# Optimization experiments

Hardware: AMD Instinct MI355X
Metric: run time of the kernel (lower is better)

## Reference

```python
import jax, jax.numpy as jnp
import numpy as np

N, D, K = 40000, 64, 16
E = N * K
EPS = 1e-5  # torch BatchNorm1d default eps


def _bn(h, g, b):
    # BatchNorm1d in training mode: biased batch statistics over dim 0
    m = h.mean(0)
    v = h.var(0)
    return (h - m) * jax.lax.rsqrt(v + EPS) * g + b


def setup_inputs() -> dict:
    key = jax.random.key(0)
    ks = jax.random.split(key, 4)
    kp = jax.random.split(ks[3], 9)

    def w(k, shape):
        return (jax.random.normal(k, shape, dtype=jnp.float32) / np.float32(np.sqrt(shape[0])))

    src = jax.random.randint(ks[2], (E,), 0, N, dtype=jnp.int32)
    dst = jnp.repeat(jnp.arange(N, dtype=jnp.int32), K)  # kNN-style: each node has K in-edges

    return {
        "x": jax.random.normal(ks[0], (N, D), dtype=jnp.float32),
        "pos": jax.random.normal(ks[1], (N, 3), dtype=jnp.float32),
        "edge_index": jnp.stack([src, dst]),
        "W_in": w(kp[0], (D, D)),
        "g1": jnp.ones(D), "b1": jnp.zeros(D),
        "W_v": w(kp[1], (D, D)),
        "W_src": w(kp[2], (D, D)),
        "W_dst": w(kp[3], (D, D)),
        "Wp1": w(kp[4], (3, 3)), "bp1": jnp.zeros(3),
        "gp": jnp.ones(3), "bp": jnp.zeros(3),
        "Wp2": w(kp[5], (3, D)), "bp2": jnp.zeros(D),
        "ga0": jnp.ones(D), "ba0": jnp.zeros(D),
        "Wa1": w(kp[6], (D, D // 8)), "ba1": jnp.zeros(D // 8),
        "ga1": jnp.ones(D // 8), "bb1": jnp.zeros(D // 8),
        "Wa2": w(kp[7], (D // 8, D)), "ba2": jnp.zeros(D),
        "g2": jnp.ones(D), "b2": jnp.zeros(D),
        "W_out": w(kp[8], (D, D)),
        "g3": jnp.ones(D), "b3": jnp.zeros(D),
    }


def reference(x, pos, edge_index, W_in, g1, b1, W_v, W_src, W_dst,
              Wp1, bp1, gp, bp, Wp2, bp2, ga0, ba0, Wa1, ba1, ga1, bb1,
              Wa2, ba2, g2, b2, W_out, g3, b3):
    src, dst = edge_index[0], edge_index[1]  # j (source), i (dest)
    n = x.shape[0]
    x_skip = x
    h = jax.nn.relu(_bn(x @ W_in, g1, b1))

    # PointTransformerConv
    a_src = h @ W_src            # alpha_j projection [N,D]
    a_dst = h @ W_dst            # alpha_i projection [N,D]
    v = h @ W_v                  # value projection  [N,D]
    rel = pos[dst] - pos[src]    # pos_i - pos_j     [E,3]
    ph = jax.nn.relu(_bn(rel @ Wp1 + bp1, gp, bp))
    delta = ph @ Wp2 + bp2       # pos_nn output     [E,D]
    a = a_dst[dst] - a_src[src] + delta
    # attn_nn: BN -> ReLU -> (Lin+BN+ReLU) -> Lin
    a = jax.nn.relu(_bn(a, ga0, ba0))
    a = jax.nn.relu(_bn(a @ Wa1 + ba1, ga1, bb1))
    a = a @ Wa2 + ba2            # [E,D]
    # segment-wise softmax over incoming edges of each dest node
    amax = jax.lax.stop_gradient(jax.ops.segment_max(a, dst, num_segments=n))
    e = jnp.exp(a - amax[dst])
    s = jax.ops.segment_sum(e, dst, num_segments=n)
    attn = e / (s[dst] + 1e-16)  # PyG softmax adds 1e-16
    agg = jax.ops.segment_sum(attn * (v[src] + delta), dst, num_segments=n)

    h = jax.nn.relu(_bn(agg, g2, b2))
    h = _bn(h @ W_out, g3, b3)
    return jax.nn.relu(h + x_skip)
```

## Files before the change

kernel.cpp:

```cpp
#include <hip/hip_runtime.h>

#define NN 40000
#define DDIM 64
#define KE 16
#define EE 640000
#define BNEPS 1e-5f

__device__ __forceinline__ void bn_coeff(const float* __restrict__ S, int C, int c,
                                         const float* __restrict__ g, const float* __restrict__ b,
                                         float inv_n, float& sc, float& sh)
{
    float m   = S[c] * inv_n;
    float var = S[C + c] * inv_n - m * m;
    float r   = rsqrtf(var + BNEPS);
    sc = g[c] * r;
    sh = b[c] - m * sc;
}

template<int TRN>
__global__ __launch_bounds__(256) void gemm64_k(
    const float* __restrict__ in,
    const float* __restrict__ W0, const float* __restrict__ W1, const float* __restrict__ W2,
    float* __restrict__ out0, float* __restrict__ out1, float* __restrict__ out2,
    const float* __restrict__ Sin, const float* __restrict__ gamma, const float* __restrict__ beta,
    float inv_n, float* __restrict__ Sout)
{
    const float* W = (blockIdx.y == 0) ? W0 : ((blockIdx.y == 1) ? W1 : W2);
    float* out     = (blockIdx.y == 0) ? out0 : ((blockIdx.y == 1) ? out1 : out2);

    __shared__ float Wl[64][64];
    __shared__ float inl[64][65];
    __shared__ float scl[64], shl[64];
    __shared__ float ssum[64], ssq[64];

    const int t = threadIdx.x;
    if (t < 64) {
        if (TRN) { float sc, sh; bn_coeff(Sin, 64, t, gamma, beta, inv_n, sc, sh); scl[t] = sc; shl[t] = sh; }
        ssum[t] = 0.f; ssq[t] = 0.f;
    }
#pragma unroll
    for (int i = 0; i < 16; i++) { int idx = t + i * 256; Wl[idx >> 6][idx & 63] = W[idx]; }
    __syncthreads();

    const int rbase = blockIdx.x * 64;
    {
        const int d = t & 63;
        float sc = 0.f, sh = 0.f;
        if (TRN) { sc = scl[d]; sh = shl[d]; }
#pragma unroll
        for (int i = 0; i < 16; i++) {
            int r = (t >> 6) + i * 4;
            float v = in[(size_t)(rbase + r) * 64 + d];
            if (TRN) v = fmaxf(fmaf(v, sc, sh), 0.f);
            inl[r][d] = v;
        }
    }
    __syncthreads();

    const int c0 = (t & 15) * 4, r0 = (t >> 4) * 4;
    float acc[4][4] = {};
#pragma unroll 16
    for (int d = 0; d < 64; d++) {
        float4 w4 = *(const float4*)&Wl[d][c0];
#pragma unroll
        for (int i = 0; i < 4; i++) {
            float h = inl[r0 + i][d];
            acc[i][0] = fmaf(h, w4.x, acc[i][0]);
            acc[i][1] = fmaf(h, w4.y, acc[i][1]);
            acc[i][2] = fmaf(h, w4.z, acc[i][2]);
            acc[i][3] = fmaf(h, w4.w, acc[i][3]);
        }
    }
#pragma unroll
    for (int i = 0; i < 4; i++) {
        float4 o; o.x = acc[i][0]; o.y = acc[i][1]; o.z = acc[i][2]; o.w = acc[i][3];
        *(float4*)&out[(size_t)(rbase + r0 + i) * 64 + c0] = o;
    }
    if (Sout) {
#pragma unroll
        for (int j = 0; j < 4; j++) {
            float s  = acc[0][j] + acc[1][j] + acc[2][j] + acc[3][j];
            float qv = acc[0][j] * acc[0][j] + acc[1][j] * acc[1][j] + acc[2][j] * acc[2][j] + acc[3][j] * acc[3][j];
            atomicAdd(&ssum[c0 + j], s);
            atomicAdd(&ssq[c0 + j], qv);
        }
        __syncthreads();
        if (t < 64) { atomicAdd(&Sout[t], ssum[t]); atomicAdd(&Sout[64 + t], ssq[t]); }
    }
}

__global__ __launch_bounds__(256) void edge_q_k(
    const float* __restrict__ pos, const int* __restrict__ src,
    const float* __restrict__ Wp1, const float* __restrict__ bp1,
    float4* __restrict__ q4, float* __restrict__ Sq)
{
    float w00 = Wp1[0], w01 = Wp1[1], w02 = Wp1[2];
    float w10 = Wp1[3], w11 = Wp1[4], w12 = Wp1[5];
    float w20 = Wp1[6], w21 = Wp1[7], w22 = Wp1[8];
    float c0 = bp1[0], c1 = bp1[1], c2 = bp1[2];
    float s0 = 0, s1 = 0, s2 = 0, p0 = 0, p1 = 0, p2 = 0;
    for (int e = blockIdx.x * blockDim.x + threadIdx.x; e < EE; e += gridDim.x * blockDim.x) {
        int sj = src[e]; int di = e >> 4;
        float r0 = pos[di * 3 + 0] - pos[sj * 3 + 0];
        float r1 = pos[di * 3 + 1] - pos[sj * 3 + 1];
        float r2 = pos[di * 3 + 2] - pos[sj * 3 + 2];
        float v0 = c0 + r0 * w00 + r1 * w10 + r2 * w20;
        float v1 = c1 + r0 * w01 + r1 * w11 + r2 * w21;
        float v2 = c2 + r0 * w02 + r1 * w12 + r2 * w22;
        float4 o; o.x = v0; o.y = v1; o.z = v2; o.w = __int_as_float(sj);
        q4[e] = o;
        s0 += v0; s1 += v1; s2 += v2;
        p0 += v0 * v0; p1 += v1 * v1; p2 += v2 * v2;
    }
#pragma unroll
    for (int o = 32; o > 0; o >>= 1) {
        s0 += __shfl_down(s0, o); s1 += __shfl_down(s1, o); s2 += __shfl_down(s2, o);
        p0 += __shfl_down(p0, o); p1 += __shfl_down(p1, o); p2 += __shfl_down(p2, o);
    }
    __shared__ float sred[4][6];
    const int w = threadIdx.x >> 6;
    if ((threadIdx.x & 63) == 0) {
        sred[w][0] = s0; sred[w][1] = s1; sred[w][2] = s2;
        sred[w][3] = p0; sred[w][4] = p1; sred[w][5] = p2;
    }
    __syncthreads();
    if (threadIdx.x < 6) {
        float v = sred[0][threadIdx.x] + sred[1][threadIdx.x] + sred[2][threadIdx.x] + sred[3][threadIdx.x];
        atomicAdd(&Sq[threadIdx.x], v);
    }
}

__global__ __launch_bounds__(256) void edge_a0_k(
    const float4* __restrict__ q4v,
    const float* __restrict__ adst, const float* __restrict__ asrc,
    const float* __restrict__ Wp2, const float* __restrict__ bp2,
    const float* __restrict__ Sq, const float* __restrict__ gp, const float* __restrict__ bp_,
    float* __restrict__ Sa0)
{
    const int lane = threadIdx.x & 63;
    const int r = lane >> 4, fq = lane & 15;
    const int wv   = blockIdx.x * (blockDim.x >> 6) + (threadIdx.x >> 6);
    const int nwv  = gridDim.x * (blockDim.x >> 6);
    const float inv_e = 1.0f / (float)EE;
    float sc30, sh30, sc31, sh31, sc32, sh32;
    bn_coeff(Sq, 3, 0, gp, bp_, inv_e, sc30, sh30);
    bn_coeff(Sq, 3, 1, gp, bp_, inv_e, sc31, sh31);
    bn_coeff(Sq, 3, 2, gp, bp_, inv_e, sc32, sh32);
    float4 w0_4 = *(const float4*)&Wp2[fq * 4];
    float4 w1_4 = *(const float4*)&Wp2[64 + fq * 4];
    float4 w2_4 = *(const float4*)&Wp2[128 + fq * 4];
    float4 bd4  = *(const float4*)&bp2[fq * 4];
    float4 s4 = {0.f,0.f,0.f,0.f}, p4 = {0.f,0.f,0.f,0.f};

    for (int i = wv; i < NN; i += nwv) {
        const int e0 = i << 4;
        float4 ad4 = *(const float4*)&adst[(size_t)i * 64 + fq * 4];
        float4 qs  = q4v[e0 + (lane & 15)];
        int sv = __float_as_int(qs.w);
        int sj[4];
#pragma unroll
        for (int p = 0; p < 4; p++) sj[p] = __shfl(sv, p * 4 + r);
        float4 av[4];
#pragma unroll
        for (int p = 0; p < 4; p++) av[p] = *(const float4*)&asrc[(size_t)sj[p] * 64 + fq * 4];
#pragma unroll
        for (int p = 0; p < 4; p++) {
            int j = p * 4 + r;
            float ph0 = fmaxf(fmaf(__shfl(qs.x, j), sc30, sh30), 0.f);
            float ph1 = fmaxf(fmaf(__shfl(qs.y, j), sc31, sh31), 0.f);
            float ph2 = fmaxf(fmaf(__shfl(qs.z, j), sc32, sh32), 0.f);
            float4 a0v;
            a0v.x = ad4.x - av[p].x + bd4.x + ph0 * w0_4.x + ph1 * w1_4.x + ph2 * w2_4.x;
            a0v.y = ad4.y - av[p].y + bd4.y + ph0 * w0_4.y + ph1 * w1_4.y + ph2 * w2_4.y;
            a0v.z = ad4.z - av[p].z + bd4.z + ph0 * w0_4.z + ph1 * w1_4.z + ph2 * w2_4.z;
            a0v.w = ad4.w - av[p].w + bd4.w + ph0 * w0_4.w + ph1 * w1_4.w + ph2 * w2_4.w;
            s4.x += a0v.x; s4.y += a0v.y; s4.z += a0v.z; s4.w += a0v.w;
            p4.x = fmaf(a0v.x, a0v.x, p4.x); p4.y = fmaf(a0v.y, a0v.y, p4.y);
            p4.z = fmaf(a0v.z, a0v.z, p4.z); p4.w = fmaf(a0v.w, a0v.w, p4.w);
        }
    }
    s4.x += __shfl_xor(s4.x, 16); s4.y += __shfl_xor(s4.y, 16);
    s4.z += __shfl_xor(s4.z, 16); s4.w += __shfl_xor(s4.w, 16);
    p4.x += __shfl_xor(p4.x, 16); p4.y += __shfl_xor(p4.y, 16);
    p4.z += __shfl_xor(p4.z, 16); p4.w += __shfl_xor(p4.w, 16);
    s4.x += __shfl_xor(s4.x, 32); s4.y += __shfl_xor(s4.y, 32);
    s4.z += __shfl_xor(s4.z, 32); s4.w += __shfl_xor(s4.w, 32);
    p4.x += __shfl_xor(p4.x, 32); p4.y += __shfl_xor(p4.y, 32);
    p4.z += __shfl_xor(p4.z, 32); p4.w += __shfl_xor(p4.w, 32);

    __shared__ float ls[64], lq[64];
    if (threadIdx.x < 64) { ls[threadIdx.x] = 0.f; lq[threadIdx.x] = 0.f; }
    __syncthreads();
    if (lane < 16) {
        atomicAdd(&ls[fq * 4 + 0], s4.x); atomicAdd(&ls[fq * 4 + 1], s4.y);
        atomicAdd(&ls[fq * 4 + 2], s4.z); atomicAdd(&ls[fq * 4 + 3], s4.w);
        atomicAdd(&lq[fq * 4 + 0], p4.x); atomicAdd(&lq[fq * 4 + 1], p4.y);
        atomicAdd(&lq[fq * 4 + 2], p4.z); atomicAdd(&lq[fq * 4 + 3], p4.w);
    }
    __syncthreads();
    if (threadIdx.x < 64) { atomicAdd(&Sa0[threadIdx.x], ls[threadIdx.x]); atomicAdd(&Sa0[64 + threadIdx.x], lq[threadIdx.x]); }
}

__global__ __launch_bounds__(256) void edge_t_k(
    const float4* __restrict__ q4v,
    const float* __restrict__ adst, const float* __restrict__ asrc,
    const float* __restrict__ Wp2, const float* __restrict__ bp2,
    const float* __restrict__ Sq, const float* __restrict__ gp, const float* __restrict__ bp_,
    const float* __restrict__ Sa0, const float* __restrict__ ga0, const float* __restrict__ ba0,
    const float* __restrict__ Wa1, const float* __restrict__ ba1,
    float* __restrict__ tout, float* __restrict__ St)
{
    __shared__ float t_l[4][16][8];
    __shared__ float red[16];
    const int t = threadIdx.x, lane = t & 63, w = t >> 6;
    const int r = lane >> 4, fq = lane & 15;
    const int wv  = blockIdx.x * 4 + w;
    const int nwv = gridDim.x * 4;
    const float inv_e = 1.0f / (float)EE;
    float sc30, sh30, sc31, sh31, sc32, sh32;
    bn_coeff(Sq, 3, 0, gp, bp_, inv_e, sc30, sh30);
    bn_coeff(Sq, 3, 1, gp, bp_, inv_e, sc31, sh31);
    bn_coeff(Sq, 3, 2, gp, bp_, inv_e, sc32, sh32);
    float4 scA4, shA4;
    bn_coeff(Sa0, 64, fq * 4 + 0, ga0, ba0, inv_e, scA4.x, shA4.x);
    bn_coeff(Sa0, 64, fq * 4 + 1, ga0, ba0, inv_e, scA4.y, shA4.y);
    bn_coeff(Sa0, 64, fq * 4 + 2, ga0, ba0, inv_e, scA4.z, shA4.z);
    bn_coeff(Sa0, 64, fq * 4 + 3, ga0, ba0, inv_e, scA4.w, shA4.w);
    float4 w0_4 = *(const float4*)&Wp2[fq * 4];
    float4 w1_4 = *(const float4*)&Wp2[64 + fq * 4];
    float4 w2_4 = *(const float4*)&Wp2[128 + fq * 4];
    float4 bd4  = *(const float4*)&bp2[fq * 4];
    float wAf[4][8];
#pragma unroll
    for (int d = 0; d < 4; d++) {
        float4 lo = *(const float4*)&Wa1[(size_t)(fq * 4 + d) * 8];
        float4 hi = *(const float4*)&Wa1[(size_t)(fq * 4 + d) * 8 + 4];
        wAf[d][0] = lo.x; wAf[d][1] = lo.y; wAf[d][2] = lo.z; wAf[d][3] = lo.w;
        wAf[d][4] = hi.x; wAf[d][5] = hi.y; wAf[d][6] = hi.z; wAf[d][7] = hi.w;
    }
    float bb[8];
    {
        float4 lo = *(const float4*)&ba1[0];
        float4 hi = *(const float4*)&ba1[4];
        bb[0] = lo.x; bb[1] = lo.y; bb[2] = lo.z; bb[3] = lo.w;
        bb[4] = hi.x; bb[5] = hi.y; bb[6] = hi.z; bb[7] = hi.w;
    }
    float ss[8] = {}, sp[8] = {};
    if (t < 16) red[t] = 0.f;
    __syncthreads();

    for (int i = wv; i < NN; i += nwv) {
        const int e0 = i << 4;
        float4 ad4 = *(const float4*)&adst[(size_t)i * 64 + fq * 4];
        float4 qs  = q4v[e0 + (lane & 15)];
        int sv = __float_as_int(qs.w);
        int sj[4];
#pragma unroll
        for (int p = 0; p < 4; p++) sj[p] = __shfl(sv, p * 4 + r);
        float4 av[4];
#pragma unroll
        for (int p = 0; p < 4; p++) av[p] = *(const float4*)&asrc[(size_t)sj[p] * 64 + fq * 4];
#pragma unroll
        for (int p = 0; p < 4; p++) {
            int j = p * 4 + r;
            float ph0 = fmaxf(fmaf(__shfl(qs.x, j), sc30, sh30), 0.f);
            float ph1 = fmaxf(fmaf(__shfl(qs.y, j), sc31, sh31), 0.f);
            float ph2 = fmaxf(fmaf(__shfl(qs.z, j), sc32, sh32), 0.f);
            float4 a1v;
            a1v.x = ad4.x - av[p].x + bd4.x + ph0 * w0_4.x + ph1 * w1_4.x + ph2 * w2_4.x;
            a1v.y = ad4.y - av[p].y + bd4.y + ph0 * w0_4.y + ph1 * w1_4.y + ph2 * w2_4.y;
            a1v.z = ad4.z - av[p].z + bd4.z + ph0 * w0_4.z + ph1 * w1_4.z + ph2 * w2_4.z;
            a1v.w = ad4.w - av[p].w + bd4.w + ph0 * w0_4.w + ph1 * w1_4.w + ph2 * w2_4.w;
            a1v.x = fmaxf(fmaf(a1v.x, scA4.x, shA4.x), 0.f);
            a1v.y = fmaxf(fmaf(a1v.y, scA4.y, shA4.y), 0.f);
            a1v.z = fmaxf(fmaf(a1v.z, scA4.z, shA4.z), 0.f);
            a1v.w = fmaxf(fmaf(a1v.w, scA4.w, shA4.w), 0.f);
            float part[8];
#pragma unroll
            for (int k = 0; k < 8; k++) {
                part[k] = a1v.x * wAf[0][k] + a1v.y * wAf[1][k]
                        + a1v.z * wAf[2][k] + a1v.w * wAf[3][k];
            }
#pragma unroll
            for (int k = 0; k < 8; k++) {
                part[k] += __shfl_xor(part[k], 1);
                part[k] += __shfl_xor(part[k], 2);
                part[k] += __shfl_xor(part[k], 4);
                part[k] += __shfl_xor(part[k], 8);
            }
            if (fq == 0) {
#pragma unroll
                for (int k = 0; k < 8; k++) {
                    float v = part[k] + bb[k];
                    t_l[w][p * 4 + r][k] = v;
                    ss[k] += v; sp[k] = fmaf(v, v, sp[k]);
                }
            }
        }
        float2 o = *(const float2*)&t_l[w][lane >> 2][(lane & 3) * 2];
        *(float2*)&tout[(size_t)e0 * 8 + lane * 2] = o;
    }
#pragma unroll
    for (int k = 0; k < 8; k++) {
        ss[k] += __shfl_xor(ss[k], 16); ss[k] += __shfl_xor(ss[k], 32);
        sp[k] += __shfl_xor(sp[k], 16); sp[k] += __shfl_xor(sp[k], 32);
    }
    if (lane == 0) {
#pragma unroll
        for (int k = 0; k < 8; k++) { atomicAdd(&red[k], ss[k]); atomicAdd(&red[8 + k], sp[k]); }
    }
    __syncthreads();
    if (t < 16) atomicAdd(&St[t], red[t]);
}

__global__ __launch_bounds__(256) void edge_final_k(
    const float* __restrict__ tin,
    const float4* __restrict__ q4v, const float* __restrict__ vv,
    const float* __restrict__ Wp2, const float* __restrict__ bp2,
    const float* __restrict__ Sq, const float* __restrict__ gp, const float* __restrict__ bp_,
    const float* __restrict__ St, const float* __restrict__ ga1, const float* __restrict__ bb1,
    const float* __restrict__ Wa2, const float* __restrict__ ba2,
    float* __restrict__ agg, float* __restrict__ Sagg)
{
    __shared__ float att_l[4][16][68];
    __shared__ float tt_l[4][16][8];
    __shared__ float ls[64], lq[64];
    const int t = threadIdx.x, lane = t & 63, w = t >> 6;
    const int r = lane >> 4, fq = lane & 15;
    const float inv_e = 1.0f / (float)EE;
    float sc3[3], sh3[3];
#pragma unroll
    for (int k = 0; k < 3; k++) bn_coeff(Sq, 3, k, gp, bp_, inv_e, sc3[k], sh3[k]);
    float sc8[8], sh8[8];
#pragma unroll
    for (int k = 0; k < 8; k++) bn_coeff(St, 8, k, ga1, bb1, inv_e, sc8[k], sh8[k]);
    float wa[8];
#pragma unroll
    for (int k = 0; k < 8; k++) wa[k] = Wa2[k * 64 + lane];
    float bad = ba2[lane];
    float4 wp0_4 = *(const float4*)&Wp2[fq * 4];
    float4 wp1_4 = *(const float4*)&Wp2[64 + fq * 4];
    float4 wp2_4 = *(const float4*)&Wp2[128 + fq * 4];
    float4 bpd4  = *(const float4*)&bp2[fq * 4];
    float4 ssum4 = {0.f, 0.f, 0.f, 0.f}, ssq4 = {0.f, 0.f, 0.f, 0.f};

    for (int nn = 0; nn < 4; nn++) {
        const int i  = blockIdx.x * 16 + nn * 4 + w;
        const int e0 = i << 4;
        if (lane < 32) {
            float4 v = *(const float4*)&tin[(size_t)e0 * 8 + lane * 4];
            ((float4*)&tt_l[w][0][0])[lane] = v;
        }
        float4 qs = q4v[e0 + (lane & 15)];
        int sv = __float_as_int(qs.w);
        __syncthreads();
        {
            float ax[16];
            float m = -3.0e38f;
#pragma unroll
            for (int j = 0; j < 16; j++) {
                float4 ta = *(const float4*)&tt_l[w][j][0];
                float4 tb = *(const float4*)&tt_l[w][j][4];
                float a = bad;
                a = fmaf(fmaxf(fmaf(ta.x, sc8[0], sh8[0]), 0.f), wa[0], a);
                a = fmaf(fmaxf(fmaf(ta.y, sc8[1], sh8[1]), 0.f), wa[1], a);
                a = fmaf(fmaxf(fmaf(ta.z, sc8[2], sh8[2]), 0.f), wa[2], a);
                a = fmaf(fmaxf(fmaf(ta.w, sc8[3], sh8[3]), 0.f), wa[3], a);
                a = fmaf(fmaxf(fmaf(tb.x, sc8[4], sh8[4]), 0.f), wa[4], a);
                a = fmaf(fmaxf(fmaf(tb.y, sc8[5], sh8[5]), 0.f), wa[5], a);
                a = fmaf(fmaxf(fmaf(tb.z, sc8[6], sh8[6]), 0.f), wa[6], a);
                a = fmaf(fmaxf(fmaf(tb.w, sc8[7], sh8[7]), 0.f), wa[7], a);
                ax[j] = a; m = fmaxf(m, a);
            }
            float s = 0.f;
#pragma unroll
            for (int j = 0; j < 16; j++) { ax[j] = __expf(ax[j] - m); s += ax[j]; }
            float inv = 1.0f / (s + 1e-16f);
#pragma unroll
            for (int j = 0; j < 16; j++) att_l[w][j][lane] = ax[j] * inv;
        }
        __syncthreads();
        {
            float4 acc = {0.f, 0.f, 0.f, 0.f};
#pragma unroll
            for (int p = 0; p < 4; p++) {
                int j  = p * 4 + r;
                int sj = __shfl(sv, j);
                float4 v4  = *(const float4*)&vv[(size_t)sj * 64 + fq * 4];
                float4 at4 = *(const float4*)&att_l[w][j][fq * 4];
                float ph0 = fmaxf(fmaf(__shfl(qs.x, j), sc3[0], sh3[0]), 0.f);
                float ph1 = fmaxf(fmaf(__shfl(qs.y, j), sc3[1], sh3[1]), 0.f);
                float ph2 = fmaxf(fmaf(__shfl(qs.z, j), sc3[2], sh3[2]), 0.f);
                float4 dl4;
                dl4.x = bpd4.x + ph0 * wp0_4.x + ph1 * wp1_4.x + ph2 * wp2_4.x;
                dl4.y = bpd4.y + ph0 * wp0_4.y + ph1 * wp1_4.y + ph2 * wp2_4.y;
                dl4.z = bpd4.z + ph0 * wp0_4.z + ph1 * wp1_4.z + ph2 * wp2_4.z;
                dl4.w = bpd4.w + ph0 * wp0_4.w + ph1 * wp1_4.w + ph2 * wp2_4.w;
                acc.x = fmaf(at4.x, v4.x + dl4.x, acc.x);
                acc.y = fmaf(at4.y, v4.y + dl4.y, acc.y);
                acc.z = fmaf(at4.z, v4.z + dl4.z, acc.z);
                acc.w = fmaf(at4.w, v4.w + dl4.w, acc.w);
            }
            acc.x += __shfl_xor(acc.x, 16); acc.y += __shfl_xor(acc.y, 16);
            acc.z += __shfl_xor(acc.z, 16); acc.w += __shfl_xor(acc.w, 16);
            acc.x += __shfl_xor(acc.x, 32); acc.y += __shfl_xor(acc.y, 32);
            acc.z += __shfl_xor(acc.z, 32); acc.w += __shfl_xor(acc.w, 32);
            if (lane < 16) {
                *(float4*)&agg[(size_t)i * 64 + lane * 4] = acc;
                ssum4.x += acc.x; ssum4.y += acc.y; ssum4.z += acc.z; ssum4.w += acc.w;
                ssq4.x  += acc.x * acc.x; ssq4.y += acc.y * acc.y;
                ssq4.z  += acc.z * acc.z; ssq4.w += acc.w * acc.w;
            }
        }
        __syncthreads();
    }
    if (t < 64) { ls[t] = 0.f; lq[t] = 0.f; }
    __syncthreads();
    if (lane < 16) {
        atomicAdd(&ls[fq * 4 + 0], ssum4.x); atomicAdd(&ls[fq * 4 + 1], ssum4.y);
        atomicAdd(&ls[fq * 4 + 2], ssum4.z); atomicAdd(&ls[fq * 4 + 3], ssum4.w);
        atomicAdd(&lq[fq * 4 + 0], ssq4.x);  atomicAdd(&lq[fq * 4 + 1], ssq4.y);
        atomicAdd(&lq[fq * 4 + 2], ssq4.z);  atomicAdd(&lq[fq * 4 + 3], ssq4.w);
    }
    __syncthreads();
    if (t < 64) { atomicAdd(&Sagg[t], ls[t]); atomicAdd(&Sagg[64 + t], lq[t]); }
}

__global__ __launch_bounds__(256) void final_k(
    const float* __restrict__ t2, const float* __restrict__ x,
    const float* __restrict__ St2, const float* __restrict__ g3, const float* __restrict__ b3,
    float* __restrict__ out)
{
    __shared__ float scl[64], shl[64];
    const int t = threadIdx.x;
    if (t < 64) { float sc, sh; bn_coeff(St2, 64, t, g3, b3, 1.0f / (float)NN, sc, sh); scl[t] = sc; shl[t] = sh; }
    __syncthreads();
    int idx = blockIdx.x * 256 + t;
    int c0 = (idx & 15) * 4;
    const float4 a = *(const float4*)&t2[(size_t)idx * 4];
    const float4 b = *(const float4*)&x[(size_t)idx * 4];
    float4 o;
    o.x = fmaxf(fmaf(a.x, scl[c0 + 0], shl[c0 + 0]) + b.x, 0.f);
    o.y = fmaxf(fmaf(a.y, scl[c0 + 1], shl[c0 + 1]) + b.y, 0.f);
    o.z = fmaxf(fmaf(a.z, scl[c0 + 2], shl[c0 + 2]) + b.z, 0.f);
    o.w = fmaxf(fmaf(a.w, scl[c0 + 3], shl[c0 + 3]) + b.w, 0.f);
    *(float4*)&out[(size_t)idx * 4] = o;
}

extern "C" void kernel_launch(void* const* d_in, const int* in_sizes, int n_in,
                              void* d_out, int out_size, void* d_ws, size_t ws_size,
                              hipStream_t stream)
{
    const float* x    = (const float*)d_in[0];
    const float* pos  = (const float*)d_in[1];
    const int*   src  = (const int*)d_in[2];
    const float* W_in = (const float*)d_in[3];
    const float* g1   = (const float*)d_in[4];
    const float* b1   = (const float*)d_in[5];
    const float* W_v  = (const float*)d_in[6];
    const float* W_src= (const float*)d_in[7];
    const float* W_dst= (const float*)d_in[8];
    const float* Wp1  = (const float*)d_in[9];
    const float* bp1  = (const float*)d_in[10];
    const float* gp   = (const float*)d_in[11];
    const float* bp_  = (const float*)d_in[12];
    const float* Wp2  = (const float*)d_in[13];
    const float* bp2  = (const float*)d_in[14];
    const float* ga0  = (const float*)d_in[15];
    const float* ba0  = (const float*)d_in[16];
    const float* Wa1  = (const float*)d_in[17];
    const float* ba1  = (const float*)d_in[18];
    const float* ga1  = (const float*)d_in[19];
    const float* bb1  = (const float*)d_in[20];
    const float* Wa2  = (const float*)d_in[21];
    const float* ba2  = (const float*)d_in[22];
    const float* g2   = (const float*)d_in[23];
    const float* b2   = (const float*)d_in[24];
    const float* W_out= (const float*)d_in[25];
    const float* g3   = (const float*)d_in[26];
    const float* b3   = (const float*)d_in[27];
    float* out = (float*)d_out;

    float* wsf   = (float*)d_ws;
    float* S_t1  = wsf;
    float* S_q   = wsf + 128;
    float* S_a0  = wsf + 192;
    float* S_t   = wsf + 320;
    float* S_agg = wsf + 384;
    float* S_t2  = wsf + 512;
    const size_t N64 = (size_t)NN * 64;
    float* t1   = wsf + 1024;
    float* asrc = t1 + N64;
    float* adst = asrc + N64;
    float* vv   = adst + N64;
    float* q4   = vv + N64;
    float* tt   = q4 + 4 * (size_t)EE;
    float* agg  = t1;
    float* t2   = asrc;

    hipMemsetAsync(wsf, 0, 1024 * sizeof(float), stream);

    gemm64_k<0><<<dim3(625, 1), 256, 0, stream>>>(x, W_in, W_in, W_in, t1, t1, t1,
                                                  nullptr, nullptr, nullptr, 0.f, S_t1);
    gemm64_k<1><<<dim3(625, 3), 256, 0, stream>>>(t1, W_src, W_dst, W_v, asrc, adst, vv,
                                                  S_t1, g1, b1, 1.0f / (float)NN, nullptr);
    edge_q_k<<<256, 256, 0, stream>>>(pos, src, Wp1, bp1, (float4*)q4, S_q);
    edge_a0_k<<<2048, 256, 0, stream>>>((const float4*)q4, adst, asrc, Wp2, bp2, S_q, gp, bp_, S_a0);
    edge_t_k<<<2048, 256, 0, stream>>>((const float4*)q4, adst, asrc, Wp2, bp2, S_q, gp, bp_,
                                       S_a0, ga0, ba0, Wa1, ba1, tt, S_t);
    edge_final_k<<<2500, 256, 0, stream>>>(tt, (const float4*)q4, vv, Wp2, bp2, S_q, gp, bp_,
                                           S_t, ga1, bb1, Wa2, ba2, agg, S_agg);
    gemm64_k<1><<<dim3(625, 1), 256, 0, stream>>>(agg, W_out, W_out, W_out, t2, t2, t2,
                                                  S_agg, g2, b2, 1.0f / (float)NN, S_t2);
    final_k<<<2500, 256, 0, stream>>>(t2, x, S_t2, g3, b3, out);
}
```

Baseline: 322.4 us.

## Replace shuffle-reduction matvec with LDS staging and drop block barriers in edge kernels

In edge_t_k, each wave now writes its 16x64 post-BN activations to shared memory, and each lane computes two of the 8 outputs for one edge with a dot product over 64 inputs against Wa1, which is staged in LDS. This replaces the per-lane partial products followed by a 4-step xor-shuffle reduction on 8 values. In edge_final_k, the per-iteration __syncthreads are replaced with compiler-only memory fences, since each wave touches only its own slice of shared memory. The change relies on intra-wave lockstep for LDS visibility, which is a correctness risk because no s_waitcnt or wave barrier is guaranteed, and it adds LDS bank traffic.

```diff
diff --git a/kernel.cpp b/kernel.cpp
--- a/kernel.cpp
+++ b/kernel.cpp
@@ -5,6 +5,8 @@
 #define KE 16
 #define EE 640000
 #define BNEPS 1e-5f
+
+#define WAVE_FENCE() asm volatile("" ::: "memory")
 
 __device__ __forceinline__ void bn_coeff(const float* __restrict__ S, int C, int c,
                                          const float* __restrict__ g, const float* __restrict__ b,
@@ -210,12 +212,11 @@
     const float* __restrict__ Wa1, const float* __restrict__ ba1,
     float* __restrict__ tout, float* __restrict__ St)
 {
-    __shared__ float t_l[4][16][8];
+    __shared__ float a1l[64][68];
+    __shared__ float wl[64][8];
     __shared__ float red[16];
     const int t = threadIdx.x, lane = t & 63, w = t >> 6;
     const int r = lane >> 4, fq = lane & 15;
-    const int wv  = blockIdx.x * 4 + w;
-    const int nwv = gridDim.x * 4;
     const float inv_e = 1.0f / (float)EE;
     float sc30, sh30, sc31, sh31, sc32, sh32;
     bn_coeff(Sq, 3, 0, gp, bp_, inv_e, sc30, sh30);
@@ -230,85 +231,65 @@
     float4 w1_4 = *(const float4*)&Wp2[64 + fq * 4];
     float4 w2_4 = *(const float4*)&Wp2[128 + fq * 4];
     float4 bd4  = *(const float4*)&bp2[fq * 4];
-    float wAf[4][8];
-#pragma unroll
-    for (int d = 0; d < 4; d++) {
-        float4 lo = *(const float4*)&Wa1[(size_t)(fq * 4 + d) * 8];
-        float4 hi = *(const float4*)&Wa1[(size_t)(fq * 4 + d) * 8 + 4];
-        wAf[d][0] = lo.x; wAf[d][1] = lo.y; wAf[d][2] = lo.z; wAf[d][3] = lo.w;
-        wAf[d][4] = hi.x; wAf[d][5] = hi.y; wAf[d][6] = hi.z; wAf[d][7] = hi.w;
-    }
-    float bb[8];
-    {
-        float4 lo = *(const float4*)&ba1[0];
-        float4 hi = *(const float4*)&ba1[4];
-        bb[0] = lo.x; bb[1] = lo.y; bb[2] = lo.z; bb[3] = lo.w;
-        bb[4] = hi.x; bb[5] = hi.y; bb[6] = hi.z; bb[7] = hi.w;
-    }
-    float ss[8] = {}, sp[8] = {};
+    for (int i = t; i < 512; i += 256) wl[i >> 3][i & 7] = Wa1[i];
     if (t < 16) red[t] = 0.f;
     __syncthreads();
 
-    for (int i = wv; i < NN; i += nwv) {
+    const int eLl = lane >> 2;
+    const int j0  = (lane & 3) * 2;
+    float bA = ba1[j0], bB = ba1[j0 + 1];
+    float ssA = 0.f, spA = 0.f, ssB = 0.f, spB = 0.f;
+
+    for (int i = blockIdx.x * 4 + w; i < NN; i += gridDim.x * 4) {
         const int e0 = i << 4;
-        float4 ad4 = *(const float4*)&adst[(size_t)i * 64 + fq * 4];
-        float4 qs  = q4v[e0 + (lane & 15)];
-        int sv = __float_as_int(qs.w);
-        int sj[4];
-#pragma unroll
-        for (int p = 0; p < 4; p++) sj[p] = __shfl(sv, p * 4 + r);
-        float4 av[4];
-#pragma unroll
-        for (int p = 0; p < 4; p++) av[p] = *(const float4*)&asrc[(size_t)sj[p] * 64 + fq * 4];
-#pragma unroll
-        for (int p = 0; p < 4; p++) {
-            int j = p * 4 + r;
-            float ph0 = fmaxf(fmaf(__shfl(qs.x, j), sc30, sh30), 0.f);
-            float ph1 = fmaxf(fmaf(__shfl(qs.y, j), sc31, sh31), 0.f);
-            float ph2 = fmaxf(fmaf(__shfl(qs.z, j), sc32, sh32), 0.f);
-            float4 a1v;
-            a1v.x = ad4.x - av[p].x + bd4.x + ph0 * w0_4.x + ph1 * w1_4.x + ph2 * w2_4.x;
-            a1v.y = ad4.y - av[p].y + bd4.y + ph0 * w0_4.y + ph1 * w1_4.y + ph2 * w2_4.y;
-            a1v.z = ad4.z - av[p].z + bd4.z + ph0 * w0_4.z + ph1 * w1_4.z + ph2 * w2_4.z;
-            a1v.w = ad4.w - av[p].w + bd4.w + ph0 * w0_4.w + ph1 * w1_4.w + ph2 * w2_4.w;
-            a1v.x = fmaxf(fmaf(a1v.x, scA4.x, shA4.x), 0.f);
-            a1v.y = fmaxf(fmaf(a1v.y, scA4.y, shA4.y), 0.f);
-            a1v.z = fmaxf(fmaf(a1v.z, scA4.z, shA4.z), 0.f);
-            a1v.w = fmaxf(fmaf(a1v.w, scA4.w, shA4.w), 0.f);
-            float part[8];
-#pragma unroll
-            for (int k = 0; k < 8; k++) {
-                part[k] = a1v.x * wAf[0][k] + a1v.y * wAf[1][k]
-                        + a1v.z * wAf[2][k] + a1v.w * wAf[3][k];
+        {
+            float4 ad4 = *(const float4*)&adst[(size_t)i * 64 + fq * 4];
+            float4 qs  = q4v[e0 + (lane & 15)];
+            int sv = __float_as_int(qs.w);
+            int sj[4];
+#pragma unroll
+            for (int p = 0; p < 4; p++) sj[p] = __shfl(sv, p * 4 + r);
+            float4 av[4];
+#pragma unroll
+            for (int p = 0; p < 4; p++) av[p] = *(const float4*)&asrc[(size_t)sj[p] * 64 + fq * 4];
+#pragma unroll
+            for (int p = 0; p < 4; p++) {
+                int j = p * 4 + r;
+                float ph0 = fmaxf(fmaf(__shfl(qs.x, j), sc30, sh30), 0.f);
+                float ph1 = fmaxf(fmaf(__shfl(qs.y, j), sc31, sh31), 0.f);
+                float ph2 = fmaxf(fmaf(__shfl(qs.z, j), sc32, sh32), 0.f);
+                float4 a1v;
+                a1v.x = ad4.x - av[p].x + bd4.x + ph0 * w0_4.x + ph1 * w1_4.x + ph2 * w2_4.x;
+                a1v.y = ad4.y - av[p].y + bd4.y + ph0 * w0_4.y + ph1 * w1_4.y + ph2 * w2_4.y;
+                a1v.z = ad4.z - av[p].z + bd4.z + ph0 * w0_4.z + ph1 * w1_4.z + ph2 * w2_4.z;
+                a1v.w = ad4.w - av[p].w + bd4.w + ph0 * w0_4.w + ph1 * w1_4.w + ph2 * w2_4.w;
+                a1v.x = fmaxf(fmaf(a1v.x, scA4.x, shA4.x), 0.f);
+                a1v.y = fmaxf(fmaf(a1v.y, scA4.y, shA4.y), 0.f);
+                a1v.z = fmaxf(fmaf(a1v.z, scA4.z, shA4.z), 0.f);
+                a1v.w = fmaxf(fmaf(a1v.w, scA4.w, shA4.w), 0.f);
+                *(float4*)&a1l[w * 16 + j][fq * 4] = a1v;
             }
-#pragma unroll
-            for (int k = 0; k < 8; k++) {
-                part[k] += __shfl_xor(part[k], 1);
-                part[k] += __shfl_xor(part[k], 2);
-                part[k] += __shfl_xor(part[k], 4);
-                part[k] += __shfl_xor(part[k], 8);
+        }
+        WAVE_FENCE();
+        {
+            float acc0 = bA, acc1 = bB;
+#pragma unroll 16
+            for (int dd = 0; dd < 64; dd++) {
+                float a = a1l[w * 16 + eLl][dd];
+                acc0 = fmaf(a, wl[dd][j0], acc0);
+                acc1 = fmaf(a, wl[dd][j0 + 1], acc1);
             }
-            if (fq == 0) {
-#pragma unroll
-                for (int k = 0; k < 8; k++) {
-                    float v = part[k] + bb[k];
-                    t_l[w][p * 4 + r][k] = v;
-                    ss[k] += v; sp[k] = fmaf(v, v, sp[k]);
-                }
-            }
-        }
-        float2 o = *(const float2*)&t_l[w][lane >> 2][(lane & 3) * 2];
-        *(float2*)&tout[(size_t)e0 * 8 + lane * 2] = o;
-    }
-#pragma unroll
-    for (int k = 0; k < 8; k++) {
-        ss[k] += __shfl_xor(ss[k], 16); ss[k] += __shfl_xor(ss[k], 32);
-        sp[k] += __shfl_xor(sp[k], 16); sp[k] += __shfl_xor(sp[k], 32);
-    }
-    if (lane == 0) {
-#pragma unroll
-        for (int k = 0; k < 8; k++) { atomicAdd(&red[k], ss[k]); atomicAdd(&red[8 + k], sp[k]); }
-    }
+            int e = e0 + eLl;
+            float2 o; o.x = acc0; o.y = acc1;
+            *(float2*)&tout[(size_t)e * 8 + j0] = o;
+            ssA += acc0; spA += acc0 * acc0;
+            ssB += acc1; spB += acc1 * acc1;
+        }
+        WAVE_FENCE();
+    }
+    __syncthreads();
+    atomicAdd(&red[j0], ssA);     atomicAdd(&red[j0 + 1], ssB);
+    atomicAdd(&red[8 + j0], spA); atomicAdd(&red[8 + j0 + 1], spB);
     __syncthreads();
     if (t < 16) atomicAdd(&St[t], red[t]);
 }
@@ -353,7 +334,7 @@
         }
         float4 qs = q4v[e0 + (lane & 15)];
         int sv = __float_as_int(qs.w);
-        __syncthreads();
+        WAVE_FENCE();
         {
             float ax[16];
             float m = -3.0e38f;
@@ -379,7 +360,7 @@
 #pragma unroll
             for (int j = 0; j < 16; j++) att_l[w][j][lane] = ax[j] * inv;
         }
-        __syncthreads();
+        WAVE_FENCE();
         {
             float4 acc = {0.f, 0.f, 0.f, 0.f};
 #pragma unroll
@@ -412,7 +393,7 @@
                 ssq4.z  += acc.z * acc.z; ssq4.w += acc.w * acc.w;
             }
         }
-        __syncthreads();
+        WAVE_FENCE();
     }
     if (t < 64) { ls[t] = 0.f; lq[t] = 0.f; }
     __syncthreads();
```

New measurement: 290.9 us. 1.11x faster.
